# Kernel optimization log

Measured on AMD Instinct MI355X. Metric: run time of the kernel, lower is better.

Reference implementation:

```python
import jax, jax.numpy as jnp
import numpy as np

N_NODES = 50000
N_EDGES = 600000
F_IN = 128
HID = 128
N_GRAPHS = 512
N_CLASSES = 2


def _sage_conv(x, src, dst, Wl, Wr, b, n_nodes):
    # PyG SAGEConv (aggr='mean'): out = lin_l(mean_{j in N(i)} x_j) + lin_r(x_i)
    msg_sum = jax.ops.segment_sum(x[src], dst, num_segments=n_nodes)  # [N, F]
    deg = jax.ops.segment_sum(jnp.ones((src.shape[0],), x.dtype), dst, num_segments=n_nodes)
    agg = msg_sum / jnp.maximum(deg, 1.0)[:, None]
    return agg @ Wl + b + x @ Wr


def setup_inputs() -> dict:
    key = jax.random.key(0)
    ks = jax.random.split(key, 16)
    x = jax.random.normal(ks[0], (N_NODES, F_IN), dtype=jnp.float32)
    edge_index = jax.random.randint(ks[1], (2, N_EDGES), 0, N_NODES, dtype=jnp.int64)
    batch = jnp.sort(jax.random.randint(ks[2], (N_NODES,), 0, N_GRAPHS, dtype=jnp.int64))
    inp = {"x": x, "edge_index": edge_index, "batch": batch, "num_graphs": N_GRAPHS}
    # SAGEConv params (glorot-ish scale)
    dims = [(F_IN, HID), (HID, HID), (HID, HID), (HID, HID)]
    for i, (din, dout) in enumerate(dims, start=1):
        s = 1.0 / np.sqrt(din)
        inp[f"Wl{i}"] = jax.random.normal(ks[2 + 3 * i], (din, dout), dtype=jnp.float32) * s
        inp[f"Wr{i}"] = jax.random.normal(ks[3 + 3 * i], (din, dout), dtype=jnp.float32) * s
        inp[f"b{i}"] = jnp.zeros((dout,), dtype=jnp.float32)
    inp["Wf1"] = jax.random.normal(ks[3], (HID, 128), dtype=jnp.float32) / np.sqrt(HID)
    inp["bf1"] = jnp.zeros((128,), dtype=jnp.float32)
    inp["Wf2"] = jax.random.normal(ks[4], (128, N_CLASSES), dtype=jnp.float32) / np.sqrt(128.0)
    inp["bf2"] = jnp.zeros((N_CLASSES,), dtype=jnp.float32)
    return inp


def reference(x, edge_index, batch, num_graphs,
              Wl1, Wr1, b1, Wl2, Wr2, b2, Wl3, Wr3, b3, Wl4, Wr4, b4,
              Wf1, bf1, Wf2, bf2):
    src, dst = edge_index[0], edge_index[1]
    n = x.shape[0]
    h = jax.nn.relu(_sage_conv(x, src, dst, Wl1, Wr1, b1, n))
    h = jax.nn.relu(_sage_conv(h, src, dst, Wl2, Wr2, b2, n))
    h = jax.nn.relu(_sage_conv(h, src, dst, Wl3, Wr3, b3, n))
    h = jax.nn.relu(_sage_conv(h, src, dst, Wl4, Wr4, b4, n))
    # global_mean_pool over graphs
    pooled_sum = jax.ops.segment_sum(h, batch, num_segments=num_graphs)
    counts = jax.ops.segment_sum(jnp.ones((n,), h.dtype), batch, num_segments=num_graphs)
    pooled = pooled_sum / jnp.maximum(counts, 1.0)[:, None]
    emb = pooled @ Wf1 + bf1
    # dropout p=0.5 is identity in eval mode
    out = emb @ Wf2 + bf2
    return out
```

## Files before the change

### kernel.cpp

```cpp
#include <hip/hip_runtime.h>

#define N_NODES   50000
#define N_EDGES   600000
#define F         128
#define N_GRAPHS  512
#define MROWS     32
#define ASTRIDE   264
#define ALSTRIDE  136
#define NB_SCAN   196
#define EB        8

typedef short          short8   __attribute__((ext_vector_type(8)));
typedef float          f32x4    __attribute__((ext_vector_type(4)));
typedef unsigned int   uint4_t  __attribute__((ext_vector_type(4)));

__device__ __forceinline__ void split_bf16(float v, short& hi, short& lo) {
    unsigned u  = __float_as_uint(v);
    unsigned hb = u & 0xFFFF0000u;
    hi = (short)(u >> 16);
    float rem = v - __uint_as_float(hb);
    lo = (short)(__float_as_uint(rem) >> 16);
}

__device__ __forceinline__ unsigned short f2bf_rne(float f) {
    unsigned u = __float_as_uint(f);
    u += 0x7FFFu + ((u >> 16) & 1u);
    return (unsigned short)(u >> 16);
}

__global__ __launch_bounds__(256) void prepA_kernel(
    const float* __restrict__ x, unsigned short* __restrict__ xb,
    unsigned short* __restrict__ hb0, unsigned short* __restrict__ hb1,
    const float* __restrict__ Wl0, const float* __restrict__ Wr0,
    const float* __restrict__ Wl1, const float* __restrict__ Wr1,
    const float* __restrict__ Wl2, const float* __restrict__ Wr2,
    const float* __restrict__ Wl3, const float* __restrict__ Wr3,
    short* __restrict__ wtbase,
    const int* __restrict__ dst, int* __restrict__ cnt, int* __restrict__ pos)
{
    const int gid  = blockIdx.x * 256 + threadIdx.x;
    const int nthr = gridDim.x * 256;

    if (gid < 48) {
        int bsel = gid >> 4, c = gid & 15;
        unsigned short* p = (bsel == 0 ? xb : bsel == 1 ? hb0 : hb1)
                            + (size_t)N_NODES * F + c * 8;
        short8 z = {0,0,0,0,0,0,0,0};
        *(short8*)p = z;
    }

    for (int i = gid; i < (N_NODES * F) / 8; i += nthr) {
        float4 a = ((const float4*)x)[2 * i];
        float4 b = ((const float4*)x)[2 * i + 1];
        short8 o;
        o[0] = (short)f2bf_rne(a.x); o[1] = (short)f2bf_rne(a.y);
        o[2] = (short)f2bf_rne(a.z); o[3] = (short)f2bf_rne(a.w);
        o[4] = (short)f2bf_rne(b.x); o[5] = (short)f2bf_rne(b.y);
        o[6] = (short)f2bf_rne(b.z); o[7] = (short)f2bf_rne(b.w);
        ((short8*)xb)[i] = o;
    }

    for (int gt = gid; gt < 131072; gt += nthr) {
        int l = gt >> 15;
        int t = gt & 32767;
        const float* Wl; const float* Wr;
        switch (l) {
            case 0:  Wl = Wl0; Wr = Wr0; break;
            case 1:  Wl = Wl1; Wr = Wr1; break;
            case 2:  Wl = Wl2; Wr = Wr2; break;
            default: Wl = Wl3; Wr = Wr3; break;
        }
        int n = t >> 8, k = t & 255;
        float w = (k < F) ? Wl[k * F + n] : Wr[(k - F) * F + n];
        short h, lo;
        split_bf16(w, h, lo);
        short* hi_plane = wtbase + (size_t)l * 65536;
        hi_plane[t]         = h;
        hi_plane[32768 + t] = lo;
    }

    for (int e = gid; e < N_EDGES; e += nthr)
        pos[e] = atomicAdd(&cnt[dst[e]], 1);
}

__global__ __launch_bounds__(256) void scan2_kernel(
    const int* __restrict__ cnt,
    int* __restrict__ row_start, float* __restrict__ inv_deg)
{
    __shared__ int s[256];
    __shared__ int red[4];
    const int b = blockIdx.x, t = threadIdx.x;

    int partial = 0;
    const int lim = b * 256;
    for (int i = t; i < lim; i += 256) partial += cnt[i];
    #pragma unroll
    for (int off = 32; off > 0; off >>= 1) partial += __shfl_down(partial, off, 64);
    if ((t & 63) == 0) red[t >> 6] = partial;
    __syncthreads();
    const int boff = red[0] + red[1] + red[2] + red[3];

    int i = lim + t;
    int d = (i < N_NODES) ? cnt[i] : 0;
    s[t] = d;
    __syncthreads();
    for (int off = 1; off < 256; off <<= 1) {
        int xv  = s[t];
        int add = (t >= off) ? s[t - off] : 0;
        __syncthreads();
        s[t] = xv + add;
        __syncthreads();
    }
    int excl = s[t] - d + boff;
    if (i < N_NODES) {
        row_start[i] = excl;
        inv_deg[i]   = 1.0f / fmaxf((float)d, 1.0f);
    }
    if (b == 0 && t == 0) row_start[N_NODES] = N_EDGES;
}

__global__ void fill2_kernel(const int* __restrict__ src, const int* __restrict__ dst,
                             const int* __restrict__ row_start,
                             const int* __restrict__ pos, int* __restrict__ eidx) {
    int e = blockIdx.x * blockDim.x + threadIdx.x;
    if (e < N_EDGES)
        eidx[row_start[dst[e]] + pos[e]] = src[e];
}

__global__ __launch_bounds__(512) void layer_kernel(
    const unsigned short* __restrict__ hb_in, const int* __restrict__ row_start,
    const int* __restrict__ eidx, const float* __restrict__ inv_deg,
    const short* __restrict__ wt_hi, const short* __restrict__ wt_lo,
    const float* __restrict__ b, unsigned short* __restrict__ hb_out)
{
    __shared__ short Ahi[MROWS][ASTRIDE];
    __shared__ short Alo[MROWS][ALSTRIDE];

    const int t    = threadIdx.x;
    const int base = blockIdx.x * MROWS;

    {
        const int c8  = t & 15;
        const int rr  = t >> 4;
        const int row = base + rr;
        const bool v  = (row < N_NODES);

        int a0 = 0, na = 0;
        float sc = 0.0f;
        if (v) {
            a0 = row_start[row];
            na = row_start[row + 1] - a0;
            sc = inv_deg[row];
        }

        short8 selfv = {0,0,0,0,0,0,0,0};
        if (v) selfv = *(const short8*)(hb_in + (size_t)row * F + c8 * 8);

        float acc[8] = {0,0,0,0,0,0,0,0};
        for (int eo = 0; eo < na; eo += EB) {
            int idx[EB];
            #pragma unroll
            for (int u = 0; u < EB; ++u) {
                bool ok = (eo + u) < na;
                int  sl = ok ? a0 + eo + u : a0;
                int  ia = eidx[sl];
                idx[u] = ok ? ia : N_NODES;
            }
            #pragma unroll
            for (int u = 0; u < EB; ++u) {
                short8 hv = *(const short8*)(hb_in + (size_t)idx[u] * F + c8 * 8);
                uint4_t uw = *(const uint4_t*)&hv;
                #pragma unroll
                for (int q = 0; q < 4; ++q) {
                    unsigned wq = uw[q];
                    acc[2 * q]     += __uint_as_float(wq << 16);
                    acc[2 * q + 1] += __uint_as_float(wq & 0xFFFF0000u);
                }
            }
        }

        short8 h8, l8;
        #pragma unroll
        for (int k = 0; k < 8; ++k) {
            short h, l;
            split_bf16(acc[k] * sc, h, l);
            h8[k] = h; l8[k] = l;
        }
        *(short8*)&Ahi[rr][c8 * 8] = h8;
        *(short8*)&Alo[rr][c8 * 8] = l8;
        *(short8*)&Ahi[rr][F + c8 * 8] = selfv;
    }
    __syncthreads();

    const int w    = t >> 6;
    const int lane = t & 63;
    const int m    = lane & 15;
    const int quad = lane >> 4;
    const int n0   = w * 16 + m;

    f32x4 acc0 = {0,0,0,0};
    f32x4 acc1 = {0,0,0,0};

    #pragma unroll
    for (int ks = 0; ks < 4; ++ks) {
        const int ko = ks * 32 + quad * 8;
        short8 ah0 = *(const short8*)&Ahi[m][ko];
        short8 ah1 = *(const short8*)&Ahi[16 + m][ko];
        short8 al0 = *(const short8*)&Alo[m][ko];
        short8 al1 = *(const short8*)&Alo[16 + m][ko];
        short8 bh  = *(const short8*)&wt_hi[(size_t)n0 * 256 + ko];
        short8 bl  = *(const short8*)&wt_lo[(size_t)n0 * 256 + ko];

        acc0 = __builtin_amdgcn_mfma_f32_16x16x32_bf16(ah0, bh, acc0, 0, 0, 0);
        acc0 = __builtin_amdgcn_mfma_f32_16x16x32_bf16(ah0, bl, acc0, 0, 0, 0);
        acc0 = __builtin_amdgcn_mfma_f32_16x16x32_bf16(al0, bh, acc0, 0, 0, 0);

        acc1 = __builtin_amdgcn_mfma_f32_16x16x32_bf16(ah1, bh, acc1, 0, 0, 0);
        acc1 = __builtin_amdgcn_mfma_f32_16x16x32_bf16(ah1, bl, acc1, 0, 0, 0);
        acc1 = __builtin_amdgcn_mfma_f32_16x16x32_bf16(al1, bh, acc1, 0, 0, 0);
    }
    #pragma unroll
    for (int ks = 4; ks < 8; ++ks) {
        const int ko = ks * 32 + quad * 8;
        short8 ah0 = *(const short8*)&Ahi[m][ko];
        short8 ah1 = *(const short8*)&Ahi[16 + m][ko];
        short8 bh  = *(const short8*)&wt_hi[(size_t)n0 * 256 + ko];
        short8 bl  = *(const short8*)&wt_lo[(size_t)n0 * 256 + ko];

        acc0 = __builtin_amdgcn_mfma_f32_16x16x32_bf16(ah0, bh, acc0, 0, 0, 0);
        acc0 = __builtin_amdgcn_mfma_f32_16x16x32_bf16(ah0, bl, acc0, 0, 0, 0);

        acc1 = __builtin_amdgcn_mfma_f32_16x16x32_bf16(ah1, bh, acc1, 0, 0, 0);
        acc1 = __builtin_amdgcn_mfma_f32_16x16x32_bf16(ah1, bl, acc1, 0, 0, 0);
    }

    float bj = b[n0];
    #pragma unroll
    for (int reg = 0; reg < 4; ++reg) {
        int r0 = base + quad * 4 + reg;
        int r1 = r0 + 16;
        if (r0 < N_NODES)
            hb_out[(size_t)r0 * F + n0] = f2bf_rne(fmaxf(acc0[reg] + bj, 0.0f));
        if (r1 < N_NODES)
            hb_out[(size_t)r1 * F + n0] = f2bf_rne(fmaxf(acc1[reg] + bj, 0.0f));
    }
}

__global__ __launch_bounds__(512) void poolhead_kernel(
    const int* __restrict__ batch, const unsigned short* __restrict__ hb,
    const float* __restrict__ Wf1, const float* __restrict__ bf1,
    const float* __restrict__ Wf2, const float* __restrict__ bf2,
    float* __restrict__ out)
{
    const int g   = blockIdx.x;
    const int j   = threadIdx.x & 127;
    const int grp = threadIdx.x >> 7;

    int lo = 0, hi = N_NODES;
    while (lo < hi) { int m = (lo + hi) >> 1; if (batch[m] < g) lo = m + 1; else hi = m; }
    int start = lo;
    hi = N_NODES;
    while (lo < hi) { int m = (lo + hi) >> 1; if (batch[m] <= g) lo = m + 1; else hi = m; }
    int end = lo;

    float acc = 0.0f;
    for (int r = start + grp; r < end; r += 4)
        acc += __uint_as_float((unsigned)hb[(size_t)r * F + j] << 16);

    __shared__ float part[4][F];
    __shared__ float p[F];
    __shared__ float emb[F];
    part[grp][j] = acc;
    __syncthreads();
    if (grp == 0) {
        float tot = (part[0][j] + part[1][j]) + (part[2][j] + part[3][j]);
        p[j] = tot / fmaxf((float)(end - start), 1.0f);
    }
    __syncthreads();

    float e = 0.0f;
    #pragma unroll 8
    for (int k = grp * 32; k < grp * 32 + 32; ++k) e += p[k] * Wf1[k * F + j];
    part[grp][j] = e;
    __syncthreads();
    if (grp == 0)
        emb[j] = (part[0][j] + part[1][j]) + (part[2][j] + part[3][j]) + bf1[j];
    __syncthreads();

    if (threadIdx.x < 2) {
        float o = bf2[threadIdx.x];
        for (int k = 0; k < F; ++k) o += emb[k] * Wf2[k * 2 + threadIdx.x];
        out[(size_t)g * 2 + threadIdx.x] = o;
    }
}

extern "C" void kernel_launch(void* const* d_in, const int* in_sizes, int n_in,
                              void* d_out, int out_size, void* d_ws, size_t ws_size,
                              hipStream_t stream) {
    const float* x     = (const float*)d_in[0];
    const int*   ei    = (const int*)d_in[1];
    const int*   src   = ei;
    const int*   dst   = ei + N_EDGES;
    const int*   batch = (const int*)d_in[2];
    const float* Wl0 = (const float*)d_in[4];
    const float* Wr0 = (const float*)d_in[5];
    const float* Wl1 = (const float*)d_in[7];
    const float* Wr1 = (const float*)d_in[8];
    const float* Wl2 = (const float*)d_in[10];
    const float* Wr2 = (const float*)d_in[11];
    const float* Wl3 = (const float*)d_in[13];
    const float* Wr3 = (const float*)d_in[14];
    const float* bb[4] = {(const float*)d_in[6],  (const float*)d_in[9],
                          (const float*)d_in[12], (const float*)d_in[15]};
    const float* Wf1 = (const float*)d_in[16];
    const float* bf1 = (const float*)d_in[17];
    const float* Wf2 = (const float*)d_in[18];
    const float* bf2 = (const float*)d_in[19];
    float* out = (float*)d_out;

    const size_t HSZ = (size_t)(N_NODES + 1) * F;
    unsigned short* XB  = (unsigned short*)d_ws;
    unsigned short* HB0 = XB + HSZ;
    unsigned short* HB1 = HB0 + HSZ;
    float* inv_deg   = (float*)(HB1 + HSZ);
    int*   row_start = (int*)(inv_deg + N_NODES);
    int*   pos       = row_start + N_NODES + 1;
    int*   eidx      = pos + N_EDGES;
    int*   cnt       = eidx + N_EDGES;
    short* wtbase    = (short*)(cnt + N_NODES);

    (void)hipMemsetAsync(cnt, 0, N_NODES * sizeof(int), stream);

    prepA_kernel<<<1024, 256, 0, stream>>>(
        x, XB, HB0, HB1, Wl0, Wr0, Wl1, Wr1, Wl2, Wr2, Wl3, Wr3,
        wtbase, dst, cnt, pos);
    scan2_kernel<<<NB_SCAN, 256, 0, stream>>>(cnt, row_start, inv_deg);
    fill2_kernel<<<(N_EDGES + 255) / 256, 256, 0, stream>>>(src, dst, row_start, pos, eidx);

    const int layer_blocks = (N_NODES + MROWS - 1) / MROWS;
    const unsigned short* hin = XB;
    unsigned short* buf[2] = {HB0, HB1};
    for (int l = 0; l < 4; ++l) {
        unsigned short* tgt = buf[l & 1];
        const short* whi = wtbase + (size_t)l * 65536;
        const short* wlo = whi + 32768;
        layer_kernel<<<layer_blocks, 512, 0, stream>>>(
            hin, row_start, eidx, inv_deg, whi, wlo, bb[l], tgt);
        hin = tgt;
    }

    poolhead_kernel<<<N_GRAPHS, 512, 0, stream>>>(batch, hin, Wf1, bf1, Wf2, bf2, out);
}
```

Measured before the change: 406.2 us.

## Sort nodes by in-degree so each layer block handles similar-degree rows

Adds a degree-histogram counting sort that builds a node permutation grouped by in-degree, then makes each layer block process 32 permuted rows and scatter outputs via a shared row map. The aim is to reduce load imbalance across the 16-thread row groups inside a block, which wait for the longest neighbor list. The cost is an extra kernel, extra atomics, and scattered (non-contiguous) row reads and writes that lose locality.

```diff
diff --git a/kernel.cpp b/kernel.cpp
--- a/kernel.cpp
+++ b/kernel.cpp
@@ -9,6 +9,7 @@
 #define ALSTRIDE  136
 #define NB_SCAN   196
 #define EB        8
+#define DBINS     128
 
 typedef short          short8   __attribute__((ext_vector_type(8)));
 typedef float          f32x4    __attribute__((ext_vector_type(4)));
@@ -85,7 +86,8 @@
 
 __global__ __launch_bounds__(256) void scan2_kernel(
     const int* __restrict__ cnt,
-    int* __restrict__ row_start, float* __restrict__ inv_deg)
+    int* __restrict__ row_start, float* __restrict__ inv_deg,
+    int* __restrict__ dhist, int* __restrict__ dpos)
 {
     __shared__ int s[256];
     __shared__ int red[4];
@@ -115,8 +117,34 @@
     if (i < N_NODES) {
         row_start[i] = excl;
         inv_deg[i]   = 1.0f / fmaxf((float)d, 1.0f);
+        int bin = d < (DBINS - 1) ? d : (DBINS - 1);
+        dpos[i] = atomicAdd(&dhist[bin], 1);
     }
     if (b == 0 && t == 0) row_start[N_NODES] = N_EDGES;
+}
+
+__global__ __launch_bounds__(256) void permute_kernel(
+    const int* __restrict__ cnt, const int* __restrict__ dhist,
+    const int* __restrict__ dpos, int* __restrict__ perm)
+{
+    __shared__ int s[DBINS];
+    const int t = threadIdx.x;
+    if (t < DBINS) s[t] = dhist[t];
+    __syncthreads();
+    for (int off = 1; off < DBINS; off <<= 1) {
+        int v   = (t < DBINS) ? s[t] : 0;
+        int add = (t >= off && t < DBINS) ? s[t - off] : 0;
+        __syncthreads();
+        if (t < DBINS) s[t] = v + add;
+        __syncthreads();
+    }
+    int i = blockIdx.x * 256 + t;
+    if (i < N_NODES) {
+        int d   = cnt[i];
+        int bin = d < (DBINS - 1) ? d : (DBINS - 1);
+        int dbase = (bin == 0) ? 0 : s[bin - 1];
+        perm[dbase + dpos[i]] = i;
+    }
 }
 
 __global__ void fill2_kernel(const int* __restrict__ src, const int* __restrict__ dst,
@@ -130,20 +158,24 @@
 __global__ __launch_bounds__(512) void layer_kernel(
     const unsigned short* __restrict__ hb_in, const int* __restrict__ row_start,
     const int* __restrict__ eidx, const float* __restrict__ inv_deg,
+    const int* __restrict__ perm,
     const short* __restrict__ wt_hi, const short* __restrict__ wt_lo,
     const float* __restrict__ b, unsigned short* __restrict__ hb_out)
 {
     __shared__ short Ahi[MROWS][ASTRIDE];
     __shared__ short Alo[MROWS][ALSTRIDE];
+    __shared__ int   rowmap[MROWS];
 
     const int t    = threadIdx.x;
     const int base = blockIdx.x * MROWS;
 
     {
-        const int c8  = t & 15;
-        const int rr  = t >> 4;
-        const int row = base + rr;
-        const bool v  = (row < N_NODES);
+        const int c8   = t & 15;
+        const int rr   = t >> 4;
+        const int slot = base + rr;
+        const bool v   = (slot < N_NODES);
+        const int row  = v ? perm[slot] : N_NODES;
+        if (c8 == 0) rowmap[rr] = v ? row : -1;
 
         int a0 = 0, na = 0;
         float sc = 0.0f;
@@ -153,8 +185,7 @@
             sc = inv_deg[row];
         }
 
-        short8 selfv = {0,0,0,0,0,0,0,0};
-        if (v) selfv = *(const short8*)(hb_in + (size_t)row * F + c8 * 8);
+        short8 selfv = *(const short8*)(hb_in + (size_t)row * F + c8 * 8);
 
         float acc[8] = {0,0,0,0,0,0,0,0};
         for (int eo = 0; eo < na; eo += EB) {
@@ -237,11 +268,12 @@
     float bj = b[n0];
     #pragma unroll
     for (int reg = 0; reg < 4; ++reg) {
-        int r0 = base + quad * 4 + reg;
-        int r1 = r0 + 16;
-        if (r0 < N_NODES)
+        int s0 = quad * 4 + reg;
+        int r0 = rowmap[s0];
+        int r1 = rowmap[s0 + 16];
+        if (r0 >= 0)
             hb_out[(size_t)r0 * F + n0] = f2bf_rne(fmaxf(acc0[reg] + bj, 0.0f));
-        if (r1 < N_NODES)
+        if (r1 >= 0)
             hb_out[(size_t)r1 * F + n0] = f2bf_rne(fmaxf(acc1[reg] + bj, 0.0f));
     }
 }
@@ -327,14 +359,18 @@
     int*   pos       = row_start + N_NODES + 1;
     int*   eidx      = pos + N_EDGES;
     int*   cnt       = eidx + N_EDGES;
-    short* wtbase    = (short*)(cnt + N_NODES);
-
-    (void)hipMemsetAsync(cnt, 0, N_NODES * sizeof(int), stream);
+    int*   dhist     = cnt + N_NODES;
+    int*   dpos      = dhist + DBINS;
+    int*   perm      = dpos + N_NODES;
+    short* wtbase    = (short*)(perm + N_NODES);
+
+    (void)hipMemsetAsync(cnt, 0, (N_NODES + DBINS) * sizeof(int), stream);
 
     prepA_kernel<<<1024, 256, 0, stream>>>(
         x, XB, HB0, HB1, Wl0, Wr0, Wl1, Wr1, Wl2, Wr2, Wl3, Wr3,
         wtbase, dst, cnt, pos);
-    scan2_kernel<<<NB_SCAN, 256, 0, stream>>>(cnt, row_start, inv_deg);
+    scan2_kernel<<<NB_SCAN, 256, 0, stream>>>(cnt, row_start, inv_deg, dhist, dpos);
+    permute_kernel<<<NB_SCAN, 256, 0, stream>>>(cnt, dhist, dpos, perm);
     fill2_kernel<<<(N_EDGES + 255) / 256, 256, 0, stream>>>(src, dst, row_start, pos, eidx);
 
     const int layer_blocks = (N_NODES + MROWS - 1) / MROWS;
@@ -345,7 +381,7 @@
         const short* whi = wtbase + (size_t)l * 65536;
         const short* wlo = whi + 32768;
         layer_kernel<<<layer_blocks, 512, 0, stream>>>(
-            hin, row_start, eidx, inv_deg, whi, wlo, bb[l], tgt);
+            hin, row_start, eidx, inv_deg, perm, whi, wlo, bb[l], tgt);
         hin = tgt;
     }
 
```

Result: slower. 530.8 us (+30.7%).

## Halve layer block to 16 rows with 256 threads and drop bounds checks

Applied to the files above, without the earlier changes.

Each layer block now covers 16 node rows with 256 threads. Each wave computes two 16-column output tiles, so it reuses one A fragment against two weight fragments. Because 50000 divides evenly by 16, the row bounds checks are removed and the grid size uses exact division. This doubles the block count and makes blocks smaller, aiming for better load balance and occupancy in the gather phase, at the cost of more weight reloads per output row, since each block fetches the full weight matrix for only 16 rows.

```diff
diff --git a/kernel.cpp b/kernel.cpp
--- a/kernel.cpp
+++ b/kernel.cpp
@@ -4,7 +4,7 @@
 #define N_EDGES   600000
 #define F         128
 #define N_GRAPHS  512
-#define MROWS     32
+#define MROWS     16
 #define ASTRIDE   264
 #define ALSTRIDE  136
 #define NB_SCAN   196
@@ -127,7 +127,7 @@
         eidx[row_start[dst[e]] + pos[e]] = src[e];
 }
 
-__global__ __launch_bounds__(512) void layer_kernel(
+__global__ __launch_bounds__(256) void layer_kernel(
     const unsigned short* __restrict__ hb_in, const int* __restrict__ row_start,
     const int* __restrict__ eidx, const float* __restrict__ inv_deg,
     const short* __restrict__ wt_hi, const short* __restrict__ wt_lo,
@@ -143,18 +143,12 @@
         const int c8  = t & 15;
         const int rr  = t >> 4;
         const int row = base + rr;
-        const bool v  = (row < N_NODES);
-
-        int a0 = 0, na = 0;
-        float sc = 0.0f;
-        if (v) {
-            a0 = row_start[row];
-            na = row_start[row + 1] - a0;
-            sc = inv_deg[row];
-        }
-
-        short8 selfv = {0,0,0,0,0,0,0,0};
-        if (v) selfv = *(const short8*)(hb_in + (size_t)row * F + c8 * 8);
+
+        const int a0 = row_start[row];
+        const int na = row_start[row + 1] - a0;
+        const float sc = inv_deg[row];
+
+        short8 selfv = *(const short8*)(hb_in + (size_t)row * F + c8 * 8);
 
         float acc[8] = {0,0,0,0,0,0,0,0};
         for (int eo = 0; eo < na; eo += EB) {
@@ -196,7 +190,8 @@
     const int lane = t & 63;
     const int m    = lane & 15;
     const int quad = lane >> 4;
-    const int n0   = w * 16 + m;
+    const int n0   = w * 32 + m;
+    const int n1   = n0 + 16;
 
     f32x4 acc0 = {0,0,0,0};
     f32x4 acc1 = {0,0,0,0};
@@ -204,45 +199,44 @@
     #pragma unroll
     for (int ks = 0; ks < 4; ++ks) {
         const int ko = ks * 32 + quad * 8;
-        short8 ah0 = *(const short8*)&Ahi[m][ko];
-        short8 ah1 = *(const short8*)&Ahi[16 + m][ko];
-        short8 al0 = *(const short8*)&Alo[m][ko];
-        short8 al1 = *(const short8*)&Alo[16 + m][ko];
-        short8 bh  = *(const short8*)&wt_hi[(size_t)n0 * 256 + ko];
-        short8 bl  = *(const short8*)&wt_lo[(size_t)n0 * 256 + ko];
-
-        acc0 = __builtin_amdgcn_mfma_f32_16x16x32_bf16(ah0, bh, acc0, 0, 0, 0);
-        acc0 = __builtin_amdgcn_mfma_f32_16x16x32_bf16(ah0, bl, acc0, 0, 0, 0);
-        acc0 = __builtin_amdgcn_mfma_f32_16x16x32_bf16(al0, bh, acc0, 0, 0, 0);
-
-        acc1 = __builtin_amdgcn_mfma_f32_16x16x32_bf16(ah1, bh, acc1, 0, 0, 0);
-        acc1 = __builtin_amdgcn_mfma_f32_16x16x32_bf16(ah1, bl, acc1, 0, 0, 0);
-        acc1 = __builtin_amdgcn_mfma_f32_16x16x32_bf16(al1, bh, acc1, 0, 0, 0);
+        short8 ah  = *(const short8*)&Ahi[m][ko];
+        short8 al  = *(const short8*)&Alo[m][ko];
+        short8 bh0 = *(const short8*)&wt_hi[(size_t)n0 * 256 + ko];
+        short8 bl0 = *(const short8*)&wt_lo[(size_t)n0 * 256 + ko];
+        short8 bh1 = *(const short8*)&wt_hi[(size_t)n1 * 256 + ko];
+        short8 bl1 = *(const short8*)&wt_lo[(size_t)n1 * 256 + ko];
+
+        acc0 = __builtin_amdgcn_mfma_f32_16x16x32_bf16(ah, bh0, acc0, 0, 0, 0);
+        acc0 = __builtin_amdgcn_mfma_f32_16x16x32_bf16(ah, bl0, acc0, 0, 0, 0);
+        acc0 = __builtin_amdgcn_mfma_f32_16x16x32_bf16(al, bh0, acc0, 0, 0, 0);
+
+        acc1 = __builtin_amdgcn_mfma_f32_16x16x32_bf16(ah, bh1, acc1, 0, 0, 0);
+        acc1 = __builtin_amdgcn_mfma_f32_16x16x32_bf16(ah, bl1, acc1, 0, 0, 0);
+        acc1 = __builtin_amdgcn_mfma_f32_16x16x32_bf16(al, bh1, acc1, 0, 0, 0);
     }
     #pragma unroll
     for (int ks = 4; ks < 8; ++ks) {
         const int ko = ks * 32 + quad * 8;
-        short8 ah0 = *(const short8*)&Ahi[m][ko];
-        short8 ah1 = *(const short8*)&Ahi[16 + m][ko];
-        short8 bh  = *(const short8*)&wt_hi[(size_t)n0 * 256 + ko];
-        short8 bl  = *(const short8*)&wt_lo[(size_t)n0 * 256 + ko];
-
-        acc0 = __builtin_amdgcn_mfma_f32_16x16x32_bf16(ah0, bh, acc0, 0, 0, 0);
-        acc0 = __builtin_amdgcn_mfma_f32_16x16x32_bf16(ah0, bl, acc0, 0, 0, 0);
-
-        acc1 = __builtin_amdgcn_mfma_f32_16x16x32_bf16(ah1, bh, acc1, 0, 0, 0);
-        acc1 = __builtin_amdgcn_mfma_f32_16x16x32_bf16(ah1, bl, acc1, 0, 0, 0);
-    }
-
-    float bj = b[n0];
+        short8 ah  = *(const short8*)&Ahi[m][ko];
+        short8 bh0 = *(const short8*)&wt_hi[(size_t)n0 * 256 + ko];
+        short8 bl0 = *(const short8*)&wt_lo[(size_t)n0 * 256 + ko];
+        short8 bh1 = *(const short8*)&wt_hi[(size_t)n1 * 256 + ko];
+        short8 bl1 = *(const short8*)&wt_lo[(size_t)n1 * 256 + ko];
+
+        acc0 = __builtin_amdgcn_mfma_f32_16x16x32_bf16(ah, bh0, acc0, 0, 0, 0);
+        acc0 = __builtin_amdgcn_mfma_f32_16x16x32_bf16(ah, bl0, acc0, 0, 0, 0);
+
+        acc1 = __builtin_amdgcn_mfma_f32_16x16x32_bf16(ah, bh1, acc1, 0, 0, 0);
+        acc1 = __builtin_amdgcn_mfma_f32_16x16x32_bf16(ah, bl1, acc1, 0, 0, 0);
+    }
+
+    float b0 = b[n0];
+    float b1 = b[n1];
     #pragma unroll
     for (int reg = 0; reg < 4; ++reg) {
-        int r0 = base + quad * 4 + reg;
-        int r1 = r0 + 16;
-        if (r0 < N_NODES)
-            hb_out[(size_t)r0 * F + n0] = f2bf_rne(fmaxf(acc0[reg] + bj, 0.0f));
-        if (r1 < N_NODES)
-            hb_out[(size_t)r1 * F + n0] = f2bf_rne(fmaxf(acc1[reg] + bj, 0.0f));
+        int r = base + quad * 4 + reg;
+        hb_out[(size_t)r * F + n0] = f2bf_rne(fmaxf(acc0[reg] + b0, 0.0f));
+        hb_out[(size_t)r * F + n1] = f2bf_rne(fmaxf(acc1[reg] + b1, 0.0f));
     }
 }
 
@@ -337,14 +331,14 @@
     scan2_kernel<<<NB_SCAN, 256, 0, stream>>>(cnt, row_start, inv_deg);
     fill2_kernel<<<(N_EDGES + 255) / 256, 256, 0, stream>>>(src, dst, row_start, pos, eidx);
 
-    const int layer_blocks = (N_NODES + MROWS - 1) / MROWS;
+    const int layer_blocks = N_NODES / MROWS;
     const unsigned short* hin = XB;
     unsigned short* buf[2] = {HB0, HB1};
     for (int l = 0; l < 4; ++l) {
         unsigned short* tgt = buf[l & 1];
         const short* whi = wtbase + (size_t)l * 65536;
         const short* wlo = whi + 32768;
-        layer_kernel<<<layer_blocks, 512, 0, stream>>>(
+        layer_kernel<<<layer_blocks, 256, 0, stream>>>(
             hin, row_start, eidx, inv_deg, whi, wlo, bb[l], tgt);
         hin = tgt;
     }
```

Result: slower. 457.4 us (+12.6%).
